# Optimization experiments

Hardware: AMD Instinct MI355X
Metric: run time of the kernel (lower is better)

The kernel has to match this reference:

```python
import jax, jax.numpy as jnp
import numpy as np

D_MODEL = 1024
N_HEADS = 16
HEAD_DIM = D_MODEL // N_HEADS


def apply_rope(x):
    # x: [B, S, H, Dh]; standard rotate-half RoPE over head_dim
    B, S, H, Dh = x.shape
    inv_freq = 1.0 / (10000.0 ** (jnp.arange(0, Dh, 2, dtype=jnp.float32) / Dh))  # [Dh/2]
    pos = jnp.arange(S, dtype=jnp.float32)
    freqs = pos[:, None] * inv_freq[None, :]          # [S, Dh/2]
    cos = jnp.cos(freqs)[None, :, None, :]            # [1, S, 1, Dh/2]
    sin = jnp.sin(freqs)[None, :, None, :]
    x1, x2 = x[..., :Dh // 2], x[..., Dh // 2:]
    return jnp.concatenate([x1 * cos - x2 * sin, x1 * sin + x2 * cos], axis=-1)


def setup_inputs() -> dict:
    key = jax.random.key(0)
    ks = jax.random.split(key, 8)
    B, S, D = 2, 2048, D_MODEL
    s = 0.02
    return {
        "query": jax.random.normal(ks[0], (B, S, D), dtype=jnp.float32),
        "key": jax.random.normal(ks[1], (B, S, D), dtype=jnp.float32),
        "value": jax.random.normal(ks[2], (B, S, D), dtype=jnp.float32),
        "Wq": jax.random.normal(ks[3], (D, D), dtype=jnp.float32) * s,
        "Wk": jax.random.normal(ks[4], (D, D), dtype=jnp.float32) * s,
        "Wv": jax.random.normal(ks[5], (D, D), dtype=jnp.float32) * s,
        "Wo": jax.random.normal(ks[6], (D, D), dtype=jnp.float32) * s,
        "bo": jax.random.normal(ks[7], (D,), dtype=jnp.float32) * s,
    }


def reference(query, key, value, Wq, Wk, Wv, Wo, bo):
    B, Sq, D = query.shape
    Skv = key.shape[1]
    H, Dh = N_HEADS, HEAD_DIM
    scale = Dh ** -0.5
    # projections (torch Linear: x @ W.T)
    q = (query @ Wq.T).reshape(B, Sq, H, Dh)
    k = (key @ Wk.T).reshape(B, Skv, H, Dh)
    v = (value @ Wv.T).reshape(B, Skv, H, Dh)
    q = apply_rope(q)
    k = apply_rope(k)
    # scores: [B, H, Sq, Skv]
    scores = jnp.einsum("bqhd,bkhd->bhqk", q, k) * scale
    attn_weights = jax.nn.softmax(scores, axis=-1)
    out = jnp.einsum("bhqk,bkhd->bqhd", attn_weights, v).reshape(B, Sq, D)
    out = out @ Wo.T + bo
    return out, attn_weights
```

## Files before the change

### kernel.cpp

```cpp
#include <hip/hip_runtime.h>
#include <math.h>

#define D_MODEL 1024
#define SEQ     2048
#define NB      2
#define NH      16
#define DH      64
#define ROWS    (NB*SEQ)
#define OUT_ELEMS ((size_t)ROWS*D_MODEL)

typedef short bf16x8 __attribute__((ext_vector_type(8)));
typedef short bf16x4 __attribute__((ext_vector_type(4)));
typedef float f32x4  __attribute__((ext_vector_type(4)));

#define AS1 __attribute__((address_space(1)))
#define AS3 __attribute__((address_space(3)))

__device__ __forceinline__ float bf2f(short u){
    union{float f; unsigned v;} x; x.v = ((unsigned)(unsigned short)u) << 16; return x.f;
}
__device__ __forceinline__ short f2bf(float f){
    union{float f; unsigned v;} x; x.f = f;
    unsigned r = (x.v + 0x7FFF + ((x.v >> 16) & 1)) >> 16;
    return (short)r;
}
__device__ __forceinline__ int swz8(int row, int slot){ return slot ^ ((row + (row>>3)) & 7); }

#define MFMA16(a,b,c) __builtin_amdgcn_mfma_f32_16x16x32_bf16((a),(b),(c),0,0,0)

#define EXPSC 0.18033688011112042f

__global__ __launch_bounds__(256) void prep(const float* __restrict__ Wq,
                                            const float* __restrict__ Wk,
                                            const float* __restrict__ Wv,
                                            const float* __restrict__ Wo,
                                            const float* __restrict__ qx,
                                            const float* __restrict__ kx,
                                            const float* __restrict__ vx,
                                            short* __restrict__ wqkv,
                                            short* __restrict__ wob,
                                            short* __restrict__ xb,
                                            float* __restrict__ tab)
{
    int i = blockIdx.x*256 + threadIdx.x;
    if (i < 1048576) {
        int sel = i >> 18;
        int loc = i & 262143;
        const float* src = sel==0 ? Wq : sel==1 ? Wk : sel==2 ? Wv : Wo;
        short* dst = sel < 3 ? wqkv + (size_t)sel*1048576 : wob;
        float4 v = *(const float4*)&src[(size_t)loc*4];
        bf16x4 o = { f2bf(v.x), f2bf(v.y), f2bf(v.z), f2bf(v.w) };
        *(bf16x4*)&dst[(size_t)loc*4] = o;
    } else if (i < 4194304) {
        int e = i - 1048576;
        int sel = e >> 20;
        int loc = e & 1048575;
        const float* src = sel==0 ? qx : sel==1 ? kx : vx;
        short* dst = xb + (size_t)sel*OUT_ELEMS;
        float4 v = *(const float4*)&src[(size_t)loc*4];
        bf16x4 o = { f2bf(v.x), f2bf(v.y), f2bf(v.z), f2bf(v.w) };
        *(bf16x4*)&dst[(size_t)loc*4] = o;
    } else {
        int e = i - 4194304;
        int j = e & 31, s = e >> 5;
        float ang = (float)s * exp2f(-(float)j * 0.41524101186092437f);
        float sn, cs; sincosf(ang, &sn, &cs);
        tab[(size_t)s*64 + j*2]     = cs;
        tab[(size_t)s*64 + j*2 + 1] = sn;
    }
}

__global__ __launch_bounds__(256) void gemm_qkv(const short* __restrict__ xb,
                                                const short* __restrict__ wqkv,
                                                const float* __restrict__ tab,
                                                short* __restrict__ qb,
                                                short* __restrict__ kb,
                                                short* __restrict__ vbt)
{
    const int z = blockIdx.z;
    const short* A = xb + (size_t)z*OUT_ELEMS;
    const short* B = wqkv + (size_t)z*D_MODEL*D_MODEL;

    __shared__ __align__(16) short Alds[128*32];
    __shared__ __align__(16) short Blds[128*32];
    const int t = threadIdx.x, lane = t & 63, wid = t >> 6;
    const int m0 = blockIdx.y << 7, n0 = blockIdx.x << 7;
    const int wm = (wid >> 1) << 6, wn = (wid & 1) << 6;
    const int l15 = lane & 15, l4 = lane >> 4;

    f32x4 acc[4][4] = {};

    for (int k0 = 0; k0 < D_MODEL; k0 += 32) {
        __syncthreads();
        #pragma unroll
        for (int u = 0; u < 2; ++u) {
            int row = (wid*2 + u)*16 + (lane >> 2);
            int kc  = k0 + (lane & 3)*8;
            const short* ga = &A[(size_t)(m0 + row)*D_MODEL + kc];
            const short* gb = &B[(size_t)(n0 + row)*D_MODEL + kc];
            __builtin_amdgcn_global_load_lds((const AS1 unsigned*)ga,
                (AS3 unsigned*)&Alds[(wid*2 + u)*512], 16, 0, 0);
            __builtin_amdgcn_global_load_lds((const AS1 unsigned*)gb,
                (AS3 unsigned*)&Blds[(wid*2 + u)*512], 16, 0, 0);
        }
        __syncthreads();
        bf16x8 af[4], bfr[4];
        #pragma unroll
        for (int mf = 0; mf < 4; ++mf)
            af[mf] = *(const bf16x8*)&Alds[(wm + mf*16 + l15)*32 + l4*8];
        #pragma unroll
        for (int nf = 0; nf < 4; ++nf)
            bfr[nf] = *(const bf16x8*)&Blds[(wn + nf*16 + l15)*32 + l4*8];
        #pragma unroll
        for (int mf = 0; mf < 4; ++mf)
            #pragma unroll
            for (int nf = 0; nf < 4; ++nf)
                acc[mf][nf] = MFMA16(af[mf], bfr[nf], acc[mf][nf]);
    }

    if (z < 2) {
        short* C = z==0 ? qb : kb;
        #pragma unroll
        for (int mf = 0; mf < 4; ++mf)
            #pragma unroll
            for (int j = 0; j < 4; ++j) {
                int row = m0 + wm + mf*16 + l4*4 + j;
                int s = row & (SEQ-1);
                #pragma unroll
                for (int p = 0; p < 2; ++p) {
                    int d31 = p*16 + l15;
                    float2 cs2 = *(const float2*)&tab[(size_t)s*64 + d31*2];
                    float x1 = acc[mf][p][j], x2 = acc[mf][p+2][j];
                    size_t rb = (size_t)row*D_MODEL + n0 + wn;
                    C[rb + p*16 + l15]       = f2bf(x1*cs2.x - x2*cs2.y);
                    C[rb + (p+2)*16 + l15]   = f2bf(x1*cs2.y + x2*cs2.x);
                }
            }
    } else {
        #pragma unroll
        for (int nf = 0; nf < 4; ++nf) {
            int col = n0 + wn + nf*16 + l15;
            int hh = col >> 6, d = col & 63;
            #pragma unroll
            for (int mf = 0; mf < 4; ++mf)
                #pragma unroll
                for (int j = 0; j < 4; ++j) {
                    int row = m0 + wm + mf*16 + l4*4 + j;
                    int b = row >> 11, s = row & (SEQ-1);
                    vbt[(((size_t)(b*NH + hh))*DH + d)*SEQ + s] = f2bf(acc[mf][nf][j]);
                }
        }
    }
}

__global__ __launch_bounds__(256) void gemm_out(const short* __restrict__ A,
                                                const short* __restrict__ B,
                                                const float* __restrict__ bias,
                                                float* __restrict__ Cout)
{
    __shared__ __align__(16) short Alds[128*32];
    __shared__ __align__(16) short Blds[128*32];
    const int t = threadIdx.x, lane = t & 63, wid = t >> 6;
    const int m0 = blockIdx.y << 7, n0 = blockIdx.x << 7;
    const int wm = (wid >> 1) << 6, wn = (wid & 1) << 6;
    const int l15 = lane & 15, l4 = lane >> 4;

    f32x4 acc[4][4] = {};

    for (int k0 = 0; k0 < D_MODEL; k0 += 32) {
        __syncthreads();
        #pragma unroll
        for (int u = 0; u < 2; ++u) {
            int row = (wid*2 + u)*16 + (lane >> 2);
            int kc  = k0 + (lane & 3)*8;
            const short* ga = &A[(size_t)(m0 + row)*D_MODEL + kc];
            const short* gb = &B[(size_t)(n0 + row)*D_MODEL + kc];
            __builtin_amdgcn_global_load_lds((const AS1 unsigned*)ga,
                (AS3 unsigned*)&Alds[(wid*2 + u)*512], 16, 0, 0);
            __builtin_amdgcn_global_load_lds((const AS1 unsigned*)gb,
                (AS3 unsigned*)&Blds[(wid*2 + u)*512], 16, 0, 0);
        }
        __syncthreads();
        bf16x8 af[4], bfr[4];
        #pragma unroll
        for (int mf = 0; mf < 4; ++mf)
            af[mf] = *(const bf16x8*)&Alds[(wm + mf*16 + l15)*32 + l4*8];
        #pragma unroll
        for (int nf = 0; nf < 4; ++nf)
            bfr[nf] = *(const bf16x8*)&Blds[(wn + nf*16 + l15)*32 + l4*8];
        #pragma unroll
        for (int mf = 0; mf < 4; ++mf)
            #pragma unroll
            for (int nf = 0; nf < 4; ++nf)
                acc[mf][nf] = MFMA16(af[mf], bfr[nf], acc[mf][nf]);
    }

    #pragma unroll
    for (int nf = 0; nf < 4; ++nf) {
        int col = n0 + wn + nf*16 + l15;
        float bv = bias[col];
        #pragma unroll
        for (int mf = 0; mf < 4; ++mf)
            #pragma unroll
            for (int j = 0; j < 4; ++j) {
                int row = m0 + wm + mf*16 + l4*4 + j;
                Cout[(size_t)row*D_MODEL + col] = acc[mf][nf][j] + bv;
            }
    }
}

__global__ __launch_bounds__(512) void attn_fused(const short* __restrict__ qb,
                                                  const short* __restrict__ kb,
                                                  const short* __restrict__ vbt,
                                                  float* __restrict__ attn,
                                                  short* __restrict__ aob)
{
    __shared__ __align__(16) short Klds[2][64*64];
    __shared__ __align__(16) short Vt  [2][64*64];
    __shared__ __align__(16) short Plds[8*16*64];
    const int t = threadIdx.x, lane = t & 63, wv = t >> 6;
    const int bid = blockIdx.x;
    const int nb = (bid & 7)*64 + (bid >> 3);
    const int rb = nb & 15, bh = nb >> 4;
    const int h = bh & 15;
    const size_t bs0 = (size_t)(bh >> 4) * SEQ;
    const int qrow0 = rb << 7;
    const int l15 = lane & 15, l4 = lane >> 4;
    const int srow = t >> 3, ssl = t & 7;
    const int soff = srow*64 + swz8(srow, ssl)*8;

    bf16x8 qf[2];
    {
        int qrow = qrow0 + wv*16 + l15;
        const short* qp = &qb[(bs0 + qrow)*D_MODEL + h*DH + l4*8];
        qf[0] = *(const bf16x8*)&qp[0];
        qf[1] = *(const bf16x8*)&qp[32];
    }

    const short* kbase  = &kb[(bs0 + srow)*D_MODEL + h*DH + ssl*8];
    const short* vtbase = &vbt[((size_t)bh*DH + srow)*SEQ + ssl*8];

    float lsum = 0.f;
    {
        bf16x8 kreg = *(const bf16x8*)&kbase[0];
        *(bf16x8*)&Klds[0][soff] = kreg;
        kreg = *(const bf16x8*)&kbase[(size_t)64*D_MODEL];
        __syncthreads();
        int cur = 0;
        for (int kt = 0; kt < SEQ; kt += 64, cur ^= 1) {
            if (kt + 64 < SEQ) {
                *(bf16x8*)&Klds[cur^1][soff] = kreg;
                if (kt + 128 < SEQ)
                    kreg = *(const bf16x8*)&kbase[(size_t)(kt+128)*D_MODEL];
            }
            f32x4 sc[4] = {};
            __builtin_amdgcn_s_setprio(1);
            #pragma unroll
            for (int kk = 0; kk < 2; ++kk)
                #pragma unroll
                for (int nf = 0; nf < 4; ++nf) {
                    int krow = nf*16 + l15;
                    bf16x8 kf = *(const bf16x8*)&Klds[cur][krow*64 + swz8(krow, kk*4 + l4)*8];
                    sc[nf] = MFMA16(kf, qf[kk], sc[nf]);
                }
            __builtin_amdgcn_s_setprio(0);
            #pragma unroll
            for (int nf = 0; nf < 4; ++nf)
                #pragma unroll
                for (int j = 0; j < 4; ++j)
                    lsum += exp2f(sc[nf][j]*EXPSC);
            __syncthreads();
        }
    }
    lsum += __shfl_xor(lsum, 16);
    lsum += __shfl_xor(lsum, 32);
    const float li = 1.0f / lsum;

    f32x4 o[4] = {};
    const size_t wrow = ((size_t)bh*SEQ + qrow0 + wv*16 + l15)*SEQ;
    short* pbase = &Plds[wv*1024 + l15*64];
    {
        bf16x8 kreg = *(const bf16x8*)&kbase[0];
        bf16x8 vreg = *(const bf16x8*)&vtbase[0];
        *(bf16x8*)&Klds[0][soff] = kreg;
        *(bf16x8*)&Vt  [0][soff] = vreg;
        kreg = *(const bf16x8*)&kbase[(size_t)64*D_MODEL];
        vreg = *(const bf16x8*)&vtbase[64];
        __syncthreads();
        int cur = 0;
        for (int kt = 0; kt < SEQ; kt += 64, cur ^= 1) {
            if (kt + 64 < SEQ) {
                *(bf16x8*)&Klds[cur^1][soff] = kreg;
                *(bf16x8*)&Vt  [cur^1][soff] = vreg;
                if (kt + 128 < SEQ) {
                    kreg = *(const bf16x8*)&kbase[(size_t)(kt+128)*D_MODEL];
                    vreg = *(const bf16x8*)&vtbase[kt+128];
                }
            }
            f32x4 sc[4] = {};
            __builtin_amdgcn_s_setprio(1);
            #pragma unroll
            for (int kk = 0; kk < 2; ++kk)
                #pragma unroll
                for (int nf = 0; nf < 4; ++nf) {
                    int krow = nf*16 + l15;
                    bf16x8 kf = *(const bf16x8*)&Klds[cur][krow*64 + swz8(krow, kk*4 + l4)*8];
                    sc[nf] = MFMA16(kf, qf[kk], sc[nf]);
                }
            __builtin_amdgcn_s_setprio(0);
            #pragma unroll
            for (int nf = 0; nf < 4; ++nf) {
                float w0 = exp2f(sc[nf][0]*EXPSC) * li;
                float w1 = exp2f(sc[nf][1]*EXPSC) * li;
                float w2 = exp2f(sc[nf][2]*EXPSC) * li;
                float w3 = exp2f(sc[nf][3]*EXPSC) * li;
                f32x4 wv4 = { w0, w1, w2, w3 };
                __builtin_nontemporal_store(wv4,
                    (f32x4*)&attn[wrow + kt + nf*16 + l4*4]);
                bf16x4 pw = { f2bf(w0), f2bf(w1), f2bf(w2), f2bf(w3) };
                *(bf16x4*)&pbase[swz8(l15, nf*2 + (l4>>1))*8 + (l4&1)*4] = pw;
            }
            __builtin_amdgcn_s_setprio(1);
            #pragma unroll
            for (int kk = 0; kk < 2; ++kk) {
                bf16x8 pa = *(const bf16x8*)&pbase[swz8(l15, kk*4 + l4)*8];
                #pragma unroll
                for (int nf = 0; nf < 4; ++nf) {
                    int d = nf*16 + l15;
                    bf16x8 vf = *(const bf16x8*)&Vt[cur][d*64 + swz8(d, kk*4 + l4)*8];
                    o[nf] = MFMA16(pa, vf, o[nf]);
                }
            }
            __builtin_amdgcn_s_setprio(0);
            __syncthreads();
        }
    }
    #pragma unroll
    for (int nf = 0; nf < 4; ++nf)
        #pragma unroll
        for (int j = 0; j < 4; ++j) {
            int qr = qrow0 + wv*16 + l4*4 + j;
            aob[(bs0 + qr)*D_MODEL + h*DH + nf*16 + l15] = f2bf(o[nf][j]);
        }
}

extern "C" void kernel_launch(void* const* d_in, const int* in_sizes, int n_in,
                              void* d_out, int out_size, void* d_ws, size_t ws_size,
                              hipStream_t stream)
{
    const float* query = (const float*)d_in[0];
    const float* key_  = (const float*)d_in[1];
    const float* value = (const float*)d_in[2];
    const float* Wq    = (const float*)d_in[3];
    const float* Wk    = (const float*)d_in[4];
    const float* Wv    = (const float*)d_in[5];
    const float* Wo    = (const float*)d_in[6];
    const float* bo    = (const float*)d_in[7];

    float* out  = (float*)d_out;
    float* attn = out + OUT_ELEMS;
    short* xb   = (short*)attn;

    short* wqkv = (short*)d_ws;
    short* wob  = wqkv + (size_t)3*1048576;
    short* qb   = wob  + (size_t)1048576;
    short* kb   = qb + OUT_ELEMS;
    short* vbt  = kb + OUT_ELEMS;
    short* aob  = vbt + OUT_ELEMS;
    float* tab  = (float*)(aob + OUT_ELEMS);

    dim3 blk(256);

    hipLaunchKernelGGL(prep, dim3(16640), blk, 0, stream,
                       Wq, Wk, Wv, Wo, query, key_, value, wqkv, wob, xb, tab);
    hipLaunchKernelGGL(gemm_qkv, dim3(8, 32, 3), blk, 0, stream,
                       xb, wqkv, tab, qb, kb, vbt);
    hipLaunchKernelGGL(attn_fused, dim3(512), dim3(512), 0, stream,
                       qb, kb, vbt, attn, aob);
    hipLaunchKernelGGL(gemm_out, dim3(8, 32), blk, 0, stream, aob, wob, bo, out);
}
```

Before: 296.6 us.

## Double GEMM K-tile to 64 with XOR-swizzled LDS layout

Both the QKV and output projection GEMMs now stage K=64 slices per iteration instead of 32, halving the number of barrier pairs per K loop. The LDS layout is XOR-swizzled at 16-byte chunk granularity so the wider rows do not cause bank conflicts on the fragment reads. Shared memory per block doubles to 32 KB, which may reduce occupancy.

```diff
diff --git a/kernel.cpp b/kernel.cpp
--- a/kernel.cpp
+++ b/kernel.cpp
@@ -81,41 +81,47 @@
     const short* A = xb + (size_t)z*OUT_ELEMS;
     const short* B = wqkv + (size_t)z*D_MODEL*D_MODEL;
 
-    __shared__ __align__(16) short Alds[128*32];
-    __shared__ __align__(16) short Blds[128*32];
+    __shared__ __align__(16) short Alds[128*64];
+    __shared__ __align__(16) short Blds[128*64];
     const int t = threadIdx.x, lane = t & 63, wid = t >> 6;
     const int m0 = blockIdx.y << 7, n0 = blockIdx.x << 7;
     const int wm = (wid >> 1) << 6, wn = (wid & 1) << 6;
     const int l15 = lane & 15, l4 = lane >> 4;
+    const int gchunk = (lane & 7) ^ (lane >> 3);
+    const int rxor = l15 & 7;
 
     f32x4 acc[4][4] = {};
 
-    for (int k0 = 0; k0 < D_MODEL; k0 += 32) {
-        __syncthreads();
-        #pragma unroll
-        for (int u = 0; u < 2; ++u) {
-            int row = (wid*2 + u)*16 + (lane >> 2);
-            int kc  = k0 + (lane & 3)*8;
-            const short* ga = &A[(size_t)(m0 + row)*D_MODEL + kc];
-            const short* gb = &B[(size_t)(n0 + row)*D_MODEL + kc];
+    for (int k0 = 0; k0 < D_MODEL; k0 += 64) {
+        __syncthreads();
+        #pragma unroll
+        for (int u = 0; u < 4; ++u) {
+            int row = u*32 + wid*8 + (lane >> 3);
+            const short* ga = &A[(size_t)(m0 + row)*D_MODEL + k0 + gchunk*8];
+            const short* gb = &B[(size_t)(n0 + row)*D_MODEL + k0 + gchunk*8];
             __builtin_amdgcn_global_load_lds((const AS1 unsigned*)ga,
-                (AS3 unsigned*)&Alds[(wid*2 + u)*512], 16, 0, 0);
+                (AS3 unsigned*)&Alds[u*2048 + wid*512], 16, 0, 0);
             __builtin_amdgcn_global_load_lds((const AS1 unsigned*)gb,
-                (AS3 unsigned*)&Blds[(wid*2 + u)*512], 16, 0, 0);
-        }
-        __syncthreads();
-        bf16x8 af[4], bfr[4];
-        #pragma unroll
-        for (int mf = 0; mf < 4; ++mf)
-            af[mf] = *(const bf16x8*)&Alds[(wm + mf*16 + l15)*32 + l4*8];
-        #pragma unroll
-        for (int nf = 0; nf < 4; ++nf)
-            bfr[nf] = *(const bf16x8*)&Blds[(wn + nf*16 + l15)*32 + l4*8];
-        #pragma unroll
-        for (int mf = 0; mf < 4; ++mf)
+                (AS3 unsigned*)&Blds[u*2048 + wid*512], 16, 0, 0);
+        }
+        __syncthreads();
+        #pragma unroll
+        for (int kk = 0; kk < 2; ++kk) {
+            bf16x8 af[4], bfr[4];
+            #pragma unroll
+            for (int mf = 0; mf < 4; ++mf)
+                af[mf] = *(const bf16x8*)&Alds[(wm + mf*16 + l15)*64
+                                               + ((kk*4 + l4) ^ rxor)*8];
             #pragma unroll
             for (int nf = 0; nf < 4; ++nf)
-                acc[mf][nf] = MFMA16(af[mf], bfr[nf], acc[mf][nf]);
+                bfr[nf] = *(const bf16x8*)&Blds[(wn + nf*16 + l15)*64
+                                                + ((kk*4 + l4) ^ rxor)*8];
+            #pragma unroll
+            for (int mf = 0; mf < 4; ++mf)
+                #pragma unroll
+                for (int nf = 0; nf < 4; ++nf)
+                    acc[mf][nf] = MFMA16(af[mf], bfr[nf], acc[mf][nf]);
+        }
     }
 
     if (z < 2) {
@@ -158,41 +164,47 @@
                                                 const float* __restrict__ bias,
                                                 float* __restrict__ Cout)
 {
-    __shared__ __align__(16) short Alds[128*32];
-    __shared__ __align__(16) short Blds[128*32];
+    __shared__ __align__(16) short Alds[128*64];
+    __shared__ __align__(16) short Blds[128*64];
     const int t = threadIdx.x, lane = t & 63, wid = t >> 6;
     const int m0 = blockIdx.y << 7, n0 = blockIdx.x << 7;
     const int wm = (wid >> 1) << 6, wn = (wid & 1) << 6;
     const int l15 = lane & 15, l4 = lane >> 4;
+    const int gchunk = (lane & 7) ^ (lane >> 3);
+    const int rxor = l15 & 7;
 
     f32x4 acc[4][4] = {};
 
-    for (int k0 = 0; k0 < D_MODEL; k0 += 32) {
-        __syncthreads();
-        #pragma unroll
-        for (int u = 0; u < 2; ++u) {
-            int row = (wid*2 + u)*16 + (lane >> 2);
-            int kc  = k0 + (lane & 3)*8;
-            const short* ga = &A[(size_t)(m0 + row)*D_MODEL + kc];
-            const short* gb = &B[(size_t)(n0 + row)*D_MODEL + kc];
+    for (int k0 = 0; k0 < D_MODEL; k0 += 64) {
+        __syncthreads();
+        #pragma unroll
+        for (int u = 0; u < 4; ++u) {
+            int row = u*32 + wid*8 + (lane >> 3);
+            const short* ga = &A[(size_t)(m0 + row)*D_MODEL + k0 + gchunk*8];
+            const short* gb = &B[(size_t)(n0 + row)*D_MODEL + k0 + gchunk*8];
             __builtin_amdgcn_global_load_lds((const AS1 unsigned*)ga,
-                (AS3 unsigned*)&Alds[(wid*2 + u)*512], 16, 0, 0);
+                (AS3 unsigned*)&Alds[u*2048 + wid*512], 16, 0, 0);
             __builtin_amdgcn_global_load_lds((const AS1 unsigned*)gb,
-                (AS3 unsigned*)&Blds[(wid*2 + u)*512], 16, 0, 0);
-        }
-        __syncthreads();
-        bf16x8 af[4], bfr[4];
-        #pragma unroll
-        for (int mf = 0; mf < 4; ++mf)
-            af[mf] = *(const bf16x8*)&Alds[(wm + mf*16 + l15)*32 + l4*8];
-        #pragma unroll
-        for (int nf = 0; nf < 4; ++nf)
-            bfr[nf] = *(const bf16x8*)&Blds[(wn + nf*16 + l15)*32 + l4*8];
-        #pragma unroll
-        for (int mf = 0; mf < 4; ++mf)
+                (AS3 unsigned*)&Blds[u*2048 + wid*512], 16, 0, 0);
+        }
+        __syncthreads();
+        #pragma unroll
+        for (int kk = 0; kk < 2; ++kk) {
+            bf16x8 af[4], bfr[4];
+            #pragma unroll
+            for (int mf = 0; mf < 4; ++mf)
+                af[mf] = *(const bf16x8*)&Alds[(wm + mf*16 + l15)*64
+                                               + ((kk*4 + l4) ^ rxor)*8];
             #pragma unroll
             for (int nf = 0; nf < 4; ++nf)
-                acc[mf][nf] = MFMA16(af[mf], bfr[nf], acc[mf][nf]);
+                bfr[nf] = *(const bf16x8*)&Blds[(wn + nf*16 + l15)*64
+                                                + ((kk*4 + l4) ^ rxor)*8];
+            #pragma unroll
+            for (int mf = 0; mf < 4; ++mf)
+                #pragma unroll
+                for (int nf = 0; nf < 4; ++nf)
+                    acc[mf][nf] = MFMA16(af[mf], bfr[nf], acc[mf][nf]);
+        }
     }
 
     #pragma unroll
```

New measurement: 291.8 us. Within noise of the previous version (-1.6%).
